# Kernel optimization log

Measured on AMD Instinct MI355X. Metric: run time of the kernel, lower is better.

The kernel has to match this reference:

```python
import jax, jax.numpy as jnp
import numpy as np


def _bag_mean(idx, table):
    # F.embedding_bag(mode='mean', padding_idx=last row): padding entries are
    # excluded from both the sum and the count. idx: [B, S, K]
    pad = table.shape[0] - 1
    mask = (idx != pad)[..., None].astype(table.dtype)          # [B,S,K,1]
    emb = table[idx] * mask                                      # [B,S,K,D]
    cnt = mask.sum(axis=-2)                                      # [B,S,1]
    s = emb.sum(axis=-2)                                         # [B,S,D]
    return jnp.where(cnt > 0, s / jnp.maximum(cnt, 1.0), 0.0)


def _subgraph_parts(qq, ques_table, skill_table, diff_table, area_table,
                    ques2skill, ques2diff, ques2area):
    qe = ques_table[qq]                                          # [B,S,D]
    sk = _bag_mean(ques2skill[qq], skill_table)                  # [B,S,D]
    df = diff_table[ques2diff[qq][..., 0]]                       # [B,S,D]
    ar = area_table[ques2area[qq][..., 0]]                       # [B,S,D]
    return qe, sk, df, ar


def reference(q, a, next_q, ques_table, skill_table, diff_table, area_table,
              ques2skill, ques2diff, ques2area, Wq, bq):
    # ---- get_subgraph_embedding (non-JunYi path) ----
    qe, sk, df, ar = _subgraph_parts(q, ques_table, skill_table, diff_table,
                                     area_table, ques2skill, ques2diff, ques2area)
    q_emb = (qe + sk + df + ar) / 4.0

    nqe, nsk, ndf, nar = _subgraph_parts(next_q, ques_table, skill_table,
                                         diff_table, area_table, ques2skill,
                                         ques2diff, ques2area)
    nq_emb = (nqe + nsk + ndf + nar) / 4.0
    # faithful to source: the averaging line for next_q is applied twice
    nq_emb = (nq_emb + nsk + ndf + nar) / 4.0

    q_emb = q_emb @ Wq.T + bq
    nq_emb = nq_emb @ Wq.T + bq

    # ---- Fusion_Module: answer==1 keeps first half, answer==0 keeps second ----
    af = a[..., None].astype(q_emb.dtype)                        # [B,S,1]
    input_emb = jnp.concatenate([q_emb * af, q_emb * (1.0 - af)], axis=-1)

    return jnp.concatenate([input_emb, nq_emb], axis=-1)        # [B,S,3D]


def setup_inputs() -> dict:
    key = jax.random.key(0)
    ks = jax.random.split(key, 12)
    B, S, D = 16, 2048, 128
    NQ, NS, ND, NA, K = 200001, 2001, 100, 50, 8
    return {
        "q": jax.random.randint(ks[0], (B, S), 0, NQ - 1),
        "a": jax.random.randint(ks[1], (B, S), 0, 2),
        "next_q": jax.random.randint(ks[2], (B, S), 0, NQ - 1),
        "ques_table": jax.random.normal(ks[3], (NQ, D), jnp.float32),
        "skill_table": jax.random.normal(ks[4], (NS, D), jnp.float32),
        "diff_table": jax.random.normal(ks[5], (ND, D), jnp.float32),
        "area_table": jax.random.normal(ks[6], (NA, D), jnp.float32),
        "ques2skill": jax.random.randint(ks[7], (NQ, K), 0, NS),
        "ques2diff": jax.random.randint(ks[8], (NQ, 1), 0, ND),
        "ques2area": jax.random.randint(ks[9], (NQ, 1), 0, NA),
        "Wq": jax.random.normal(ks[10], (D, D), jnp.float32) / np.sqrt(D),
        "bq": jax.random.normal(ks[11], (D,), jnp.float32) * 0.01,
    }
```

## Files before the change

kernel.cpp:

```cpp
#include <hip/hip_runtime.h>
#include <hip/hip_bf16.h>

typedef float  f32x4  __attribute__((ext_vector_type(4)));
typedef short  s16x8  __attribute__((ext_vector_type(8)));

__device__ __forceinline__ unsigned short f2bf(float f) {
    unsigned int u = __float_as_uint(f);
    unsigned int rnd = 0x7fffu + ((u >> 16) & 1u);
    return (unsigned short)((u + rnd) >> 16);
}

__device__ __forceinline__ void bf8_fma(const s16x8 v, float s, f32x4& a0, f32x4& a1) {
    const uint4 u = *(const uint4*)&v;
    a0[0] += s * __uint_as_float(u.x << 16);
    a0[1] += s * __uint_as_float(u.x & 0xffff0000u);
    a0[2] += s * __uint_as_float(u.y << 16);
    a0[3] += s * __uint_as_float(u.y & 0xffff0000u);
    a1[0] += s * __uint_as_float(u.z << 16);
    a1[1] += s * __uint_as_float(u.z & 0xffff0000u);
    a1[2] += s * __uint_as_float(u.w << 16);
    a1[3] += s * __uint_as_float(u.w & 0xffff0000u);
}

__global__ __launch_bounds__(256)
void h2kt_prep(const float* __restrict__ Wq,
               const float* __restrict__ skill, const float* __restrict__ diff,
               const float* __restrict__ area,
               const int* __restrict__ q, const int* __restrict__ next_q,
               const int* __restrict__ a_arr,
               const int* __restrict__ q2s, const int* __restrict__ q2d,
               const int* __restrict__ q2a,
               unsigned short* __restrict__ Wqb,
               unsigned short* __restrict__ T2,
               int* __restrict__ desc,
               int pad_idx)
{
    const int bid = blockIdx.x, tid = threadIdx.x;

    if (bid < 8) {
        const int s  = bid * 256 + tid;
        const int f  = s >> 6, sl = s & 63;
        const int jt = f >> 2, kt = f & 3;
        const int row = jt * 16 + (sl & 15);
        const int col = kt * 32 + (sl >> 4) * 8;
        const float4 w0 = *(const float4*)(Wq + row * 128 + col);
        const float4 w1 = *(const float4*)(Wq + row * 128 + col + 4);
        s16x8 v;
        v[0] = (short)f2bf(w0.x); v[1] = (short)f2bf(w0.y);
        v[2] = (short)f2bf(w0.z); v[3] = (short)f2bf(w0.w);
        v[4] = (short)f2bf(w1.x); v[5] = (short)f2bf(w1.y);
        v[6] = (short)f2bf(w1.z); v[7] = (short)f2bf(w1.w);
        *(s16x8*)(Wqb + (size_t)s * 8) = v;
    } else if (bid < 42) {
        const int lane = tid & 63;
        const int cl = lane & 15, grp = lane >> 4;
        const int row16 = ((bid - 8) * 4 + (tid >> 6)) * 16;
        if (row16 > 2150) return;

        int srow = row16 + cl;
        if (srow > 2150) srow = 2150;
        const float* src = (srow < 2001) ? skill + (size_t)srow * 128
                         : (srow < 2101) ? diff + (size_t)(srow - 2001) * 128
                                         : area + (size_t)(srow - 2101) * 128;
        s16x8 afr[4];
        #pragma unroll
        for (int kt = 0; kt < 4; ++kt) {
            const float4 v0 = *(const float4*)(src + kt * 32 + grp * 8);
            const float4 v1 = *(const float4*)(src + kt * 32 + grp * 8 + 4);
            s16x8 v;
            v[0] = (short)f2bf(v0.x); v[1] = (short)f2bf(v0.y);
            v[2] = (short)f2bf(v0.z); v[3] = (short)f2bf(v0.w);
            v[4] = (short)f2bf(v1.x); v[5] = (short)f2bf(v1.y);
            v[6] = (short)f2bf(v1.z); v[7] = (short)f2bf(v1.w);
            afr[kt] = v;
        }
        #pragma unroll
        for (int jt = 0; jt < 8; ++jt) {
            f32x4 acc = {0.f, 0.f, 0.f, 0.f};
            #pragma unroll
            for (int kt = 0; kt < 4; ++kt) {
                const float* wp = Wq + (jt * 16 + cl) * 128 + kt * 32 + grp * 8;
                const float4 w0 = *(const float4*)(wp);
                const float4 w1 = *(const float4*)(wp + 4);
                s16x8 bf;
                bf[0] = (short)f2bf(w0.x); bf[1] = (short)f2bf(w0.y);
                bf[2] = (short)f2bf(w0.z); bf[3] = (short)f2bf(w0.w);
                bf[4] = (short)f2bf(w1.x); bf[5] = (short)f2bf(w1.y);
                bf[6] = (short)f2bf(w1.z); bf[7] = (short)f2bf(w1.w);
                acc = __builtin_amdgcn_mfma_f32_16x16x32_bf16(afr[kt], bf, acc, 0, 0, 0);
            }
            #pragma unroll
            for (int r = 0; r < 4; ++r) {
                const int orow = row16 + grp * 4 + r;
                if (orow < 2151) T2[(size_t)orow * 128 + jt * 16 + cl] = f2bf(acc[r]);
            }
        }
    } else {
        const int g = (bid - 42) * 256 + tid;
        const int p = g & 32767;
        const bool isnq = (g >= 32768);
        const int qq = isnq ? next_q[p] : q[p];
        const int4 s03 = *(const int4*)(q2s + (size_t)qq * 8);
        const int4 s47 = *(const int4*)(q2s + (size_t)qq * 8 + 4);
        const int di = q2d[qq];
        const int ai = q2a[qq];
        const int av = isnq ? 1 : a_arr[p];
        int4* d = (int4*)(desc + (size_t)g * 12);
        d[0] = make_int4(qq, s03.x, s03.y, s03.z);
        d[1] = make_int4(s03.w, s47.x, s47.y, s47.z);
        d[2] = make_int4(s47.w, 2001 + di, 2101 + ai, av);
    }
}

__global__ __launch_bounds__(256, 4)
void h2kt_fused(const int* __restrict__ desc,
                const float* __restrict__ ques_table,
                const unsigned short* __restrict__ T2,
                const unsigned short* __restrict__ Wqb,
                const float* __restrict__ bq,
                float* __restrict__ out,
                int pad_idx)
{
    __shared__ __align__(16) unsigned char U[16 * 132 * 4];
    unsigned short* Q = (unsigned short*)U;
    float*          D = (float*)U;

    const int tid  = threadIdx.x;
    const int w    = tid >> 6;
    const int lane = tid & 63;
    const int cl   = lane & 15;
    const int grp  = lane >> 4;
    const int r2   = lane >> 5;
    const int c    = lane & 31;
    const int g0   = blockIdx.x * 16;
    const int base = g0 & 32767;
    const bool isnq = (g0 >= 32768);
    const float wq_ = isnq ? 0.0625f : 0.25f;
    const float wr_ = isnq ? 0.3125f : 0.25f;

    const int myrow = w * 4 + grp;

    const int qq0 = desc[(size_t)(g0 + w * 4 + 0 + r2) * 12];
    const int qq1 = desc[(size_t)(g0 + w * 4 + 2 + r2) * 12];
    const int4* P = (const int4*)(desc + (size_t)(g0 + myrow) * 12);
    const int4 i0 = P[0], i1 = P[1], i2 = P[2];

    const f32x4 qv0 = *(const f32x4*)(ques_table + (size_t)qq0 * 128 + c * 4);
    const f32x4 qv1 = *(const f32x4*)(ques_table + (size_t)qq1 * 128 + c * 4);

    const int sa[8] = {i0.y, i0.z, i0.w, i1.x, i1.y, i1.z, i1.w, i2.x};
    const int av = i2.w;

    s16x8 t[10];
    #pragma unroll
    for (int i = 0; i < 8; ++i)
        t[i] = *(const s16x8*)(T2 + (size_t)sa[i] * 128 + cl * 8);
    t[8] = *(const s16x8*)(T2 + (size_t)i2.y * 128 + cl * 8);
    t[9] = *(const s16x8*)(T2 + (size_t)i2.z * 128 + cl * 8);

    int cnt = 0;
    #pragma unroll
    for (int i = 0; i < 8; ++i) cnt += (sa[i] != pad_idx);
    const float cs = cnt > 0 ? wr_ / (float)cnt : 0.f;

    f32x4 rA = {0,0,0,0}, rB = {0,0,0,0};
    #pragma unroll
    for (int i = 0; i < 8; ++i) bf8_fma(t[i], (sa[i] != pad_idx) ? cs : 0.f, rA, rB);
    bf8_fma(t[8], wr_, rA, rB);
    bf8_fma(t[9], wr_, rA, rB);

    {
        ushort4 o;
        o.x = f2bf(wq_ * qv0[0]); o.y = f2bf(wq_ * qv0[1]);
        o.z = f2bf(wq_ * qv0[2]); o.w = f2bf(wq_ * qv0[3]);
        *(ushort4*)(Q + (size_t)(w * 4 + 0 + r2) * 136 + c * 4) = o;
        o.x = f2bf(wq_ * qv1[0]); o.y = f2bf(wq_ * qv1[1]);
        o.z = f2bf(wq_ * qv1[2]); o.w = f2bf(wq_ * qv1[3]);
        *(ushort4*)(Q + (size_t)(w * 4 + 2 + r2) * 136 + c * 4) = o;
    }

    __syncthreads();

    s16x8 afr[4];
    #pragma unroll
    for (int kt = 0; kt < 4; ++kt)
        afr[kt] = *(const s16x8*)(Q + (size_t)cl * 136 + kt * 32 + grp * 8);

    __syncthreads();

    #pragma unroll
    for (int jt2 = 0; jt2 < 2; ++jt2) {
        const int jt = w * 2 + jt2;
        f32x4 acc = {0.f, 0.f, 0.f, 0.f};
        #pragma unroll
        for (int kt = 0; kt < 4; ++kt) {
            const s16x8 bf = *(const s16x8*)(Wqb + ((size_t)(jt * 4 + kt) * 64 + lane) * 8);
            acc = __builtin_amdgcn_mfma_f32_16x16x32_bf16(afr[kt], bf, acc, 0, 0, 0);
        }
        #pragma unroll
        for (int r = 0; r < 4; ++r)
            D[(size_t)(grp * 4 + r) * 132 + jt * 16 + cl] = acc[r];
    }

    __syncthreads();

    const f32x4 bq0 = *(const f32x4*)(bq + cl * 8);
    const f32x4 bq1 = *(const f32x4*)(bq + cl * 8 + 4);
    const f32x4 z = {0.f, 0.f, 0.f, 0.f};
    {
        const f32x4 d0 = *(const f32x4*)(D + (size_t)myrow * 132 + cl * 8);
        const f32x4 d1 = *(const f32x4*)(D + (size_t)myrow * 132 + cl * 8 + 4);
        const f32x4 v0 = d0 + rA + bq0;
        const f32x4 v1 = d1 + rB + bq1;
        const size_t orow = (size_t)(base + myrow);
        if (!isnq) {
            const bool on = (av != 0);
            *(f32x4*)(out + orow * 384 + cl * 8)           = on ? v0 : z;
            *(f32x4*)(out + orow * 384 + cl * 8 + 4)       = on ? v1 : z;
            *(f32x4*)(out + orow * 384 + 128 + cl * 8)     = on ? z : v0;
            *(f32x4*)(out + orow * 384 + 128 + cl * 8 + 4) = on ? z : v1;
        } else {
            *(f32x4*)(out + orow * 384 + 256 + cl * 8)     = v0;
            *(f32x4*)(out + orow * 384 + 256 + cl * 8 + 4) = v1;
        }
    }
}

extern "C" void kernel_launch(void* const* d_in, const int* in_sizes, int n_in,
                              void* d_out, int out_size, void* d_ws, size_t ws_size,
                              hipStream_t stream) {
    const int*   q          = (const int*)d_in[0];
    const int*   a          = (const int*)d_in[1];
    const int*   next_q     = (const int*)d_in[2];
    const float* ques_table = (const float*)d_in[3];
    const float* skill_tab  = (const float*)d_in[4];
    const float* diff_tab   = (const float*)d_in[5];
    const float* area_tab   = (const float*)d_in[6];
    const int*   q2s        = (const int*)d_in[7];
    const int*   q2d        = (const int*)d_in[8];
    const int*   q2a        = (const int*)d_in[9];
    const float* Wq         = (const float*)d_in[10];
    const float* bq         = (const float*)d_in[11];
    float* out = (float*)d_out;

    const int NS = in_sizes[4] / 128;
    const int pad_idx = NS - 1;

    int*            descp = (int*)d_ws;
    unsigned short* Wqb   = (unsigned short*)((char*)d_ws + (size_t)65536 * 48);
    unsigned short* T2    = Wqb + (size_t)2048 * 8;

    h2kt_prep<<<298, 256, 0, stream>>>(Wq, skill_tab, diff_tab, area_tab,
                                       q, next_q, a, q2s, q2d, q2a,
                                       Wqb, T2, descp, pad_idx);
    h2kt_fused<<<4096, 256, 0, stream>>>(descp, ques_table, T2, Wqb, bq, out, pad_idx);
}
```

Baseline: 39.80 us.

## Use 512-thread blocks with one row per half-wave in fused kernel

New measurement: 41.33 us. 3.8% more time.

```diff
diff --git a/kernel.cpp b/kernel.cpp
--- a/kernel.cpp
+++ b/kernel.cpp
@@ -3,6 +3,9 @@
 
 typedef float  f32x4  __attribute__((ext_vector_type(4)));
 typedef short  s16x8  __attribute__((ext_vector_type(8)));
+typedef short  s16x4  __attribute__((ext_vector_type(4)));
+
+#define PIN_LOADS() asm volatile("" ::: "memory")
 
 __device__ __forceinline__ unsigned short f2bf(float f) {
     unsigned int u = __float_as_uint(f);
@@ -10,16 +13,12 @@
     return (unsigned short)((u + rnd) >> 16);
 }
 
-__device__ __forceinline__ void bf8_fma(const s16x8 v, float s, f32x4& a0, f32x4& a1) {
-    const uint4 u = *(const uint4*)&v;
-    a0[0] += s * __uint_as_float(u.x << 16);
-    a0[1] += s * __uint_as_float(u.x & 0xffff0000u);
-    a0[2] += s * __uint_as_float(u.y << 16);
-    a0[3] += s * __uint_as_float(u.y & 0xffff0000u);
-    a1[0] += s * __uint_as_float(u.z << 16);
-    a1[1] += s * __uint_as_float(u.z & 0xffff0000u);
-    a1[2] += s * __uint_as_float(u.w << 16);
-    a1[3] += s * __uint_as_float(u.w & 0xffff0000u);
+__device__ __forceinline__ void bf4_fma(const s16x4 v, float s, f32x4& a) {
+    const uint2 u = *(const uint2*)&v;
+    a[0] += s * __uint_as_float(u.x << 16);
+    a[1] += s * __uint_as_float(u.x & 0xffff0000u);
+    a[2] += s * __uint_as_float(u.y << 16);
+    a[3] += s * __uint_as_float(u.y & 0xffff0000u);
 }
 
 __global__ __launch_bounds__(256)
@@ -112,7 +111,7 @@
     }
 }
 
-__global__ __launch_bounds__(256, 4)
+__global__ __launch_bounds__(512, 8)
 void h2kt_fused(const int* __restrict__ desc,
                 const float* __restrict__ ques_table,
                 const unsigned short* __restrict__ T2,
@@ -130,7 +129,7 @@
     const int lane = tid & 63;
     const int cl   = lane & 15;
     const int grp  = lane >> 4;
-    const int r2   = lane >> 5;
+    const int r    = lane >> 5;
     const int c    = lane & 31;
     const int g0   = blockIdx.x * 16;
     const int base = g0 & 32767;
@@ -138,45 +137,29 @@
     const float wq_ = isnq ? 0.0625f : 0.25f;
     const float wr_ = isnq ? 0.3125f : 0.25f;
 
-    const int myrow = w * 4 + grp;
-
-    const int qq0 = desc[(size_t)(g0 + w * 4 + 0 + r2) * 12];
-    const int qq1 = desc[(size_t)(g0 + w * 4 + 2 + r2) * 12];
+    const int myrow = w * 2 + r;
+
     const int4* P = (const int4*)(desc + (size_t)(g0 + myrow) * 12);
     const int4 i0 = P[0], i1 = P[1], i2 = P[2];
-
-    const f32x4 qv0 = *(const f32x4*)(ques_table + (size_t)qq0 * 128 + c * 4);
-    const f32x4 qv1 = *(const f32x4*)(ques_table + (size_t)qq1 * 128 + c * 4);
-
+    const int qq = i0.x;
+    const int av = i2.w;
     const int sa[8] = {i0.y, i0.z, i0.w, i1.x, i1.y, i1.z, i1.w, i2.x};
-    const int av = i2.w;
-
-    s16x8 t[10];
+
+    const f32x4 qv = *(const f32x4*)(ques_table + (size_t)qq * 128 + c * 4);
+
+    s16x4 t[10];
     #pragma unroll
     for (int i = 0; i < 8; ++i)
-        t[i] = *(const s16x8*)(T2 + (size_t)sa[i] * 128 + cl * 8);
-    t[8] = *(const s16x8*)(T2 + (size_t)i2.y * 128 + cl * 8);
-    t[9] = *(const s16x8*)(T2 + (size_t)i2.z * 128 + cl * 8);
-
-    int cnt = 0;
-    #pragma unroll
-    for (int i = 0; i < 8; ++i) cnt += (sa[i] != pad_idx);
-    const float cs = cnt > 0 ? wr_ / (float)cnt : 0.f;
-
-    f32x4 rA = {0,0,0,0}, rB = {0,0,0,0};
-    #pragma unroll
-    for (int i = 0; i < 8; ++i) bf8_fma(t[i], (sa[i] != pad_idx) ? cs : 0.f, rA, rB);
-    bf8_fma(t[8], wr_, rA, rB);
-    bf8_fma(t[9], wr_, rA, rB);
+        t[i] = *(const s16x4*)(T2 + (size_t)sa[i] * 128 + c * 4);
+    t[8] = *(const s16x4*)(T2 + (size_t)i2.y * 128 + c * 4);
+    t[9] = *(const s16x4*)(T2 + (size_t)i2.z * 128 + c * 4);
+    PIN_LOADS();
 
     {
         ushort4 o;
-        o.x = f2bf(wq_ * qv0[0]); o.y = f2bf(wq_ * qv0[1]);
-        o.z = f2bf(wq_ * qv0[2]); o.w = f2bf(wq_ * qv0[3]);
-        *(ushort4*)(Q + (size_t)(w * 4 + 0 + r2) * 136 + c * 4) = o;
-        o.x = f2bf(wq_ * qv1[0]); o.y = f2bf(wq_ * qv1[1]);
-        o.z = f2bf(wq_ * qv1[2]); o.w = f2bf(wq_ * qv1[3]);
-        *(ushort4*)(Q + (size_t)(w * 4 + 2 + r2) * 136 + c * 4) = o;
+        o.x = f2bf(wq_ * qv[0]); o.y = f2bf(wq_ * qv[1]);
+        o.z = f2bf(wq_ * qv[2]); o.w = f2bf(wq_ * qv[3]);
+        *(ushort4*)(Q + (size_t)myrow * 136 + c * 4) = o;
     }
 
     __syncthreads();
@@ -188,9 +171,8 @@
 
     __syncthreads();
 
-    #pragma unroll
-    for (int jt2 = 0; jt2 < 2; ++jt2) {
-        const int jt = w * 2 + jt2;
+    {
+        const int jt = w;
         f32x4 acc = {0.f, 0.f, 0.f, 0.f};
         #pragma unroll
         for (int kt = 0; kt < 4; ++kt) {
@@ -198,31 +180,34 @@
             acc = __builtin_amdgcn_mfma_f32_16x16x32_bf16(afr[kt], bf, acc, 0, 0, 0);
         }
         #pragma unroll
-        for (int r = 0; r < 4; ++r)
-            D[(size_t)(grp * 4 + r) * 132 + jt * 16 + cl] = acc[r];
-    }
+        for (int rr = 0; rr < 4; ++rr)
+            D[(size_t)(grp * 4 + rr) * 132 + jt * 16 + cl] = acc[rr];
+    }
+
+    int cnt = 0;
+    #pragma unroll
+    for (int i = 0; i < 8; ++i) cnt += (sa[i] != pad_idx);
+    const float cs = cnt > 0 ? wr_ / (float)cnt : 0.f;
+
+    f32x4 rA = {0.f, 0.f, 0.f, 0.f};
+    #pragma unroll
+    for (int i = 0; i < 8; ++i) bf4_fma(t[i], (sa[i] != pad_idx) ? cs : 0.f, rA);
+    bf4_fma(t[8], wr_, rA);
+    bf4_fma(t[9], wr_, rA);
 
     __syncthreads();
 
-    const f32x4 bq0 = *(const f32x4*)(bq + cl * 8);
-    const f32x4 bq1 = *(const f32x4*)(bq + cl * 8 + 4);
-    const f32x4 z = {0.f, 0.f, 0.f, 0.f};
-    {
-        const f32x4 d0 = *(const f32x4*)(D + (size_t)myrow * 132 + cl * 8);
-        const f32x4 d1 = *(const f32x4*)(D + (size_t)myrow * 132 + cl * 8 + 4);
-        const f32x4 v0 = d0 + rA + bq0;
-        const f32x4 v1 = d1 + rB + bq1;
-        const size_t orow = (size_t)(base + myrow);
-        if (!isnq) {
-            const bool on = (av != 0);
-            *(f32x4*)(out + orow * 384 + cl * 8)           = on ? v0 : z;
-            *(f32x4*)(out + orow * 384 + cl * 8 + 4)       = on ? v1 : z;
-            *(f32x4*)(out + orow * 384 + 128 + cl * 8)     = on ? z : v0;
-            *(f32x4*)(out + orow * 384 + 128 + cl * 8 + 4) = on ? z : v1;
-        } else {
-            *(f32x4*)(out + orow * 384 + 256 + cl * 8)     = v0;
-            *(f32x4*)(out + orow * 384 + 256 + cl * 8 + 4) = v1;
-        }
+    const f32x4 bq4 = *(const f32x4*)(bq + c * 4);
+    const f32x4 d0  = *(const f32x4*)(D + (size_t)myrow * 132 + c * 4);
+    const f32x4 v0  = d0 + rA + bq4;
+    const f32x4 z   = {0.f, 0.f, 0.f, 0.f};
+    const size_t orow = (size_t)(base + myrow);
+    if (!isnq) {
+        const bool on = (av != 0);
+        *(f32x4*)(out + orow * 384 + c * 4)       = on ? v0 : z;
+        *(f32x4*)(out + orow * 384 + 128 + c * 4) = on ? z : v0;
+    } else {
+        *(f32x4*)(out + orow * 384 + 256 + c * 4) = v0;
     }
 }
 
@@ -253,5 +238,5 @@
     h2kt_prep<<<298, 256, 0, stream>>>(Wq, skill_tab, diff_tab, area_tab,
                                        q, next_q, a, q2s, q2d, q2a,
                                        Wqb, T2, descp, pad_idx);
-    h2kt_fused<<<4096, 256, 0, stream>>>(descp, ques_table, T2, Wqb, bq, out, pad_idx);
-}
+    h2kt_fused<<<4096, 512, 0, stream>>>(descp, ques_table, T2, Wqb, bq, out, pad_idx);
+}
```
